# Optimization experiments

Hardware: AMD Instinct MI355X
Metric: run time of the kernel (lower is better)

## Reference

```python
import jax, jax.numpy as jnp
import numpy as np

B, L, M = 32768, 128, 1024  # batch, latent_size, num_basis_function


def setup_inputs() -> dict:
    key = jax.random.key(0)
    k1, k2, k3 = jax.random.split(key, 3)
    u_lat = jax.random.normal(k1, (B, L), dtype=jnp.float32)
    centres = jax.random.normal(k2, (M, L), dtype=jnp.float32)      # RBF centres (torch init: N(0,1))
    log_sigmas = jnp.zeros((M,), dtype=jnp.float32)                  # RBF log bandwidths (torch init: 0)
    lin1_w = jax.random.normal(k3, (M,), dtype=jnp.float32) / np.float32(np.sqrt(M))  # Linear(M,1,bias=False)
    return {"u_lat": u_lat, "centres": centres, "log_sigmas": log_sigmas, "lin1_w": lin1_w}


def _V_batch(u, centres, log_sigmas, lin1_w):
    """Potential V(h) = ELU(w . multiquadric(||h-c||/sigma)) + 0.5*||h||^2, per row. Returns [B]."""
    u_sq = jnp.sum(u * u, axis=-1)                                   # [B]
    c_sq = jnp.sum(centres * centres, axis=-1)                       # [M]
    # ||h - c||^2 via norm expansion: avoids [B, M, L] intermediate
    sq_dist = jnp.maximum(u_sq[:, None] + c_sq[None, :] - 2.0 * (u @ centres.T), 0.0)  # [B, M]
    d = jnp.sqrt(sq_dist) / jnp.exp(log_sigmas)[None, :]             # [B, M]
    phi = jnp.sqrt(1.0 + d * d)                                      # multiquadric kernel
    e = jax.nn.elu(phi @ lin1_w)                                     # [B]
    return e + 0.5 * u_sq


def reference(u_lat, centres, log_sigmas, lin1_w):
    # LEBNN.forward: f_lat = dV/dh evaluated per sample (vmap(jacrev) in torch).
    # Each entry of _V_batch depends only on its own row of u_lat, so
    # grad of the summed potential gives the per-sample Jacobian rows exactly.
    grad_fn = jax.grad(lambda u: jnp.sum(_V_batch(u, centres, log_sigmas, lin1_w)))
    return grad_fn(u_lat)  # [B, L]
```

## Files before the change

### kernel.cpp

```cpp
#include <hip/hip_runtime.h>
#include <math.h>

#define B_N 32768
#define L_N 128
#define M_N 1024
#define NT 512
#define TB 64
#define TM 64
#define NCHUNK (M_N / TM)

typedef __bf16 v8bf __attribute__((ext_vector_type(8)));
typedef __bf16 v4bf __attribute__((ext_vector_type(4)));
typedef float  v4f  __attribute__((ext_vector_type(4)));
typedef float  v2f  __attribute__((ext_vector_type(2)));
typedef unsigned int u32x2 __attribute__((ext_vector_type(2)));

#define MFMA(a, b, c) __builtin_amdgcn_mfma_f32_16x16x32_bf16(a, b, c, 0, 0, 0)

#define US  136
#define CNS 136
#define QSCALE 64.0f
#define QINV   0.015625f

__device__ inline v8bf pack8(float4 a, float4 b) {
    v8bf v;
    v[0] = (__bf16)a.x; v[1] = (__bf16)a.y; v[2] = (__bf16)a.z; v[3] = (__bf16)a.w;
    v[4] = (__bf16)b.x; v[5] = (__bf16)b.y; v[6] = (__bf16)b.z; v[7] = (__bf16)b.w;
    return v;
}

__global__ void lebnn_setup(const float* __restrict__ centres,
                            const float* __restrict__ log_sigmas,
                            const float* __restrict__ lin_w,
                            float4* __restrict__ cpack,
                            __bf16* __restrict__ cT,
                            __bf16* __restrict__ cbn) {
    __shared__ __bf16 tile[64 * 72];
    const int bx = blockIdx.x;
    if (bx < 32) {
        const int m0 = (bx & 15) * 64;
        const int l0 = (bx >> 4) * 64;
        const int row = threadIdx.x >> 2;
        const int seg = threadIdx.x & 3;
        const float* src = centres + (size_t)(m0 + row) * L_N + l0 + seg * 16;
        float4 a0 = *(const float4*)(src);
        float4 a1 = *(const float4*)(src + 4);
        float4 a2 = *(const float4*)(src + 8);
        float4 a3 = *(const float4*)(src + 12);
        v8bf p0 = pack8(a0, a1);
        v8bf p1 = pack8(a2, a3);
        *(v8bf*)&tile[row * 72 + seg * 16]     = p0;
        *(v8bf*)&tile[row * 72 + seg * 16 + 8] = p1;
        __bf16* rdst = cbn + (size_t)(m0 + row) * L_N + l0 + seg * 16;
        *(v8bf*)(rdst)     = p0;
        *(v8bf*)(rdst + 8) = p1;
        __syncthreads();
        v8bf o0, o1;
#pragma unroll
        for (int i = 0; i < 8; ++i) o0[i] = tile[(seg * 16 + i) * 72 + row];
#pragma unroll
        for (int i = 0; i < 8; ++i) o1[i] = tile[(seg * 16 + 8 + i) * 72 + row];
        __bf16* dst = cT + (size_t)(l0 + row) * M_N + m0 + seg * 16;
        *(v8bf*)(dst)     = o0;
        *(v8bf*)(dst + 8) = o1;
    } else {
        int m = (bx - 32) * 256 + threadIdx.x;
        if (m < M_N) {
            const float4* row = (const float4*)(centres + (size_t)m * L_N);
            float s = 0.f;
#pragma unroll
            for (int i = 0; i < L_N / 4; ++i) {
                float4 v = row[i];
                s += v.x * v.x + v.y * v.y + v.z * v.z + v.w * v.w;
            }
            float4 p;
            p.x = s;
            p.y = expf(-2.f * log_sigmas[m]);
            p.z = lin_w[m];
            p.w = 0.f;
            cpack[m] = p;
        }
    }
}

__global__ __launch_bounds__(NT) void lebnn_phase1(
    const float* __restrict__ u, const __bf16* __restrict__ cbn,
    const float4* __restrict__ cpack, unsigned int* __restrict__ qg32,
    float* __restrict__ gg, float* __restrict__ rsg)
{
    __shared__ __bf16 u_bf[TB * US];
    __shared__ __bf16 c_n[TM * CNS];
    __shared__ float usq_s[TB];
    __shared__ float upart[TB * 9];
    __shared__ float sred[288];
    __shared__ float rred[288];

    const int tid  = threadIdx.x;
    const int w    = tid >> 6;
    const int lane = tid & 63;
    const int l15  = lane & 15;
    const int l4   = lane >> 4;
    const int bh   = w >> 2;
    const int mq   = w & 3;
    const int b0   = blockIdx.x * TB;

    {
        int row = tid >> 3, seg = tid & 7;
        const float* up = u + (size_t)(b0 + row) * L_N + seg * 16;
        float4 a0 = *(const float4*)(up);
        float4 a1 = *(const float4*)(up + 4);
        float4 a2 = *(const float4*)(up + 8);
        float4 a3 = *(const float4*)(up + 12);
        float ps = a0.x*a0.x + a0.y*a0.y + a0.z*a0.z + a0.w*a0.w
                 + a1.x*a1.x + a1.y*a1.y + a1.z*a1.z + a1.w*a1.w
                 + a2.x*a2.x + a2.y*a2.y + a2.z*a2.z + a2.w*a2.w
                 + a3.x*a3.x + a3.y*a3.y + a3.z*a3.z + a3.w*a3.w;
        *(v8bf*)&u_bf[row * US + seg * 16]     = pack8(a0, a1);
        *(v8bf*)&u_bf[row * US + seg * 16 + 8] = pack8(a2, a3);
        upart[row * 9 + seg] = ps;
    }
    __syncthreads();
    if (tid < TB) {
        float s = 0.f;
#pragma unroll
        for (int i = 0; i < 8; ++i) s += upart[tid * 9 + i];
        usq_s[tid] = s;
    }
    __syncthreads();

    v8bf uf[2][4];
#pragma unroll
    for (int bt = 0; bt < 2; ++bt)
#pragma unroll
        for (int kk = 0; kk < 4; ++kk)
            uf[bt][kk] = *(v8bf*)&u_bf[(bh*32 + bt*16 + l15) * US + kk*32 + l4*8];

    float usq_r[2][4];
#pragma unroll
    for (int bt = 0; bt < 2; ++bt)
#pragma unroll
        for (int r = 0; r < 4; ++r)
            usq_r[bt][r] = usq_s[bh*32 + bt*16 + l4*4 + r];

    float s_p[2][4] = {{0.f,0.f,0.f,0.f},{0.f,0.f,0.f,0.f}};
    float r_p[2][4] = {{0.f,0.f,0.f,0.f},{0.f,0.f,0.f,0.f}};

    const int srow = tid >> 3;
    const int sseg = tid & 7;

    for (int mt = 0; mt < NCHUNK; ++mt) {
        const int m0 = mt * TM;
        __syncthreads();
        {
            const __bf16* cp = cbn + (size_t)(m0 + srow) * L_N + sseg * 16;
            *(v8bf*)&c_n[srow * CNS + sseg * 16]     = *(const v8bf*)(cp);
            *(v8bf*)&c_n[srow * CNS + sseg * 16 + 8] = *(const v8bf*)(cp + 8);
        }
        float4 cpv = cpack[m0 + mq*16 + l15];
        __syncthreads();

        v4f dot[2];
        dot[0] = (v4f){0.f,0.f,0.f,0.f};
        dot[1] = (v4f){0.f,0.f,0.f,0.f};
#pragma unroll
        for (int kk = 0; kk < 4; ++kk) {
            v8bf bfr = *(v8bf*)&c_n[(mq*16 + l15) * CNS + kk*32 + l4*8];
            dot[0] = MFMA(uf[0][kk], bfr, dot[0]);
            dot[1] = MFMA(uf[1][kk], bfr, dot[1]);
        }

        float qs[8];
        const float wqs = cpv.z * cpv.y * QSCALE;
#pragma unroll
        for (int bt = 0; bt < 2; ++bt) {
#pragma unroll
            for (int r = 0; r < 4; ++r) {
                float dv  = dot[bt][r];
                float raw = fmaf(-2.f, dv, usq_r[bt][r] + cpv.x);
                float x   = fmaf(fmaxf(raw, 0.f), cpv.y, 1.f);
                float ri  = rsqrtf(x);
                s_p[bt][r] = fmaf(cpv.z, x * ri, s_p[bt][r]);
                float qv  = (raw > 0.f) ? wqs * ri : 0.f;
                r_p[bt][r] += qv;
                qs[bt*4 + r] = qv;
            }
        }
        unsigned int w0 = 0, w1 = 0;
        w0 = __builtin_amdgcn_cvt_pk_fp8_f32(qs[0], qs[1], w0, false);
        w0 = __builtin_amdgcn_cvt_pk_fp8_f32(qs[2], qs[3], w0, true);
        w1 = __builtin_amdgcn_cvt_pk_fp8_f32(qs[4], qs[5], w1, false);
        w1 = __builtin_amdgcn_cvt_pk_fp8_f32(qs[6], qs[7], w1, true);
        u32x2 qw; qw[0] = w0; qw[1] = w1;
        *(u32x2*)(qg32 + ((size_t)blockIdx.x * NCHUNK + mt) * (NT * 2) + tid * 2) = qw;
    }

#pragma unroll
    for (int bt = 0; bt < 2; ++bt)
#pragma unroll
        for (int r = 0; r < 4; ++r) {
#pragma unroll
            for (int msk = 1; msk < 16; msk <<= 1) {
                s_p[bt][r] += __shfl_xor(s_p[bt][r], msk, 64);
                r_p[bt][r] += __shfl_xor(r_p[bt][r], msk, 64);
            }
        }
    if (l15 == 0) {
#pragma unroll
        for (int bt = 0; bt < 2; ++bt)
#pragma unroll
            for (int r = 0; r < 4; ++r) {
                sred[w*36 + bt*16 + l4*4 + r] = s_p[bt][r];
                rred[w*36 + bt*16 + l4*4 + r] = r_p[bt][r];
            }
    }
    __syncthreads();

    if (tid < TB) {
        int bhh = tid >> 5, rowr = tid & 31;
        float s = 0.f, R = 0.f;
#pragma unroll
        for (int i = 0; i < 4; ++i) {
            s += sred[(bhh*4 + i)*36 + rowr];
            R += rred[(bhh*4 + i)*36 + rowr];
        }
        float g = (s > 0.f) ? 1.f : expf(s);
        gg[b0 + tid]  = g;
        rsg[b0 + tid] = fmaf(g * QINV, R, 1.f);
    }
}

__global__ __launch_bounds__(NT) void lebnn_gemm2(
    const float* __restrict__ u, const unsigned int* __restrict__ qg32,
    const __bf16* __restrict__ cT, const float* __restrict__ gg,
    const float* __restrict__ rsg, float* __restrict__ out)
{
    __shared__ __bf16 qt[64 * 72];
    __shared__ __bf16 ct[128 * 72];

    const int tid  = threadIdx.x;
    const int w    = tid >> 6;
    const int lane = tid & 63;
    const int l15  = lane & 15;
    const int l4   = lane >> 4;
    const int bh   = w >> 2;
    const int lq   = w & 3;
    const int bb0  = blockIdx.x * 64;
    const int lr   = tid >> 2;
    const int sg   = tid & 3;

    v4f acc[2][2];
#pragma unroll
    for (int bt = 0; bt < 2; ++bt)
#pragma unroll
        for (int lt = 0; lt < 2; ++lt)
            acc[bt][lt] = (v4f){0.f, 0.f, 0.f, 0.f};

    u32x2 qw = *(const u32x2*)(qg32 + ((size_t)blockIdx.x * NCHUNK + 0) * (NT * 2) + tid * 2);
    const __bf16* csrc = cT + (size_t)lr * M_N + sg * 16;
    v8bf cva = *(const v8bf*)(csrc);
    v8bf cvb = *(const v8bf*)(csrc + 8);

    for (int mt = 0; mt < NCHUNK; ++mt) {
        __syncthreads();
        {
            v2f p0 = __builtin_amdgcn_cvt_pk_f32_fp8(qw[0], false);
            v2f p1 = __builtin_amdgcn_cvt_pk_f32_fp8(qw[0], true);
            v2f p2 = __builtin_amdgcn_cvt_pk_f32_fp8(qw[1], false);
            v2f p3 = __builtin_amdgcn_cvt_pk_f32_fp8(qw[1], true);
            __bf16 qb[8];
            qb[0] = (__bf16)p0[0]; qb[1] = (__bf16)p0[1];
            qb[2] = (__bf16)p1[0]; qb[3] = (__bf16)p1[1];
            qb[4] = (__bf16)p2[0]; qb[5] = (__bf16)p2[1];
            qb[6] = (__bf16)p3[0]; qb[7] = (__bf16)p3[1];
#pragma unroll
            for (int bt = 0; bt < 2; ++bt)
#pragma unroll
                for (int r = 0; r < 4; ++r)
                    qt[(bh*32 + bt*16 + l4*4 + r) * 72 + lq*16 + l15] = qb[bt*4 + r];
            *(v8bf*)&ct[lr * 72 + sg * 16]     = cva;
            *(v8bf*)&ct[lr * 72 + sg * 16 + 8] = cvb;
        }
        __syncthreads();

        if (mt + 1 < NCHUNK) {
            qw = *(const u32x2*)(qg32 + ((size_t)blockIdx.x * NCHUNK + (mt+1)) * (NT * 2) + tid * 2);
            const __bf16* cn = cT + (size_t)lr * M_N + (mt+1) * TM + sg * 16;
            cva = *(const v8bf*)(cn);
            cvb = *(const v8bf*)(cn + 8);
        }

#pragma unroll
        for (int kk = 0; kk < 2; ++kk) {
            v8bf qa0 = *(v8bf*)&qt[(bh*32 +  0 + l15) * 72 + kk*32 + l4*8];
            v8bf qa1 = *(v8bf*)&qt[(bh*32 + 16 + l15) * 72 + kk*32 + l4*8];
#pragma unroll
            for (int lt = 0; lt < 2; ++lt) {
                v8bf cb = *(v8bf*)&ct[(lq*32 + lt*16 + l15) * 72 + kk*32 + l4*8];
                acc[0][lt] = MFMA(qa0, cb, acc[0][lt]);
                acc[1][lt] = MFMA(qa1, cb, acc[1][lt]);
            }
        }
    }

    float gv[2][4], rv[2][4];
#pragma unroll
    for (int bt = 0; bt < 2; ++bt)
#pragma unroll
        for (int r = 0; r < 4; ++r) {
            int b = bb0 + bh*32 + bt*16 + l4*4 + r;
            gv[bt][r] = gg[b] * QINV;
            rv[bt][r] = rsg[b];
        }
#pragma unroll
    for (int bt = 0; bt < 2; ++bt)
#pragma unroll
        for (int lt = 0; lt < 2; ++lt)
#pragma unroll
            for (int r = 0; r < 4; ++r) {
                size_t idx = (size_t)(bb0 + bh*32 + bt*16 + l4*4 + r) * L_N
                           + lq*32 + lt*16 + l15;
                out[idx] = fmaf(u[idx], rv[bt][r], -gv[bt][r] * acc[bt][lt][r]);
            }
}

#define CFS 68
#define OFF_UBF   0
#define OFF_CN    17408
#define OFF_CFL   34816
#define OFF_USQ   52224
#define OFF_UPART 52480
#define OFF_SRED  54784
#define OFF_RRED  55936
#define OFF_G     57088
#define OFF_RS    57344
#define SMEM_BYTES 57600

__global__ __launch_bounds__(NT) void lebnn_fallback(
    const float* __restrict__ u, const float* __restrict__ centres,
    const float4* __restrict__ cpack, float* __restrict__ out)
{
    extern __shared__ char smem[];
    __bf16* u_bf = (__bf16*)(smem + OFF_UBF);
    __bf16* c_n  = (__bf16*)(smem + OFF_CN);
    float*  cfl  = (float*)(smem + OFF_CFL);
    float* usq_s = (float*)(smem + OFF_USQ);
    float* upart = (float*)(smem + OFF_UPART);
    float* sred  = (float*)(smem + OFF_SRED);
    float* rred  = (float*)(smem + OFF_RRED);
    float* gsh   = (float*)(smem + OFF_G);
    float* rssh  = (float*)(smem + OFF_RS);

    const int tid  = threadIdx.x;
    const int w    = tid >> 6;
    const int lane = tid & 63;
    const int l15  = lane & 15;
    const int l4   = lane >> 4;
    const int bh   = w >> 2;
    const int mq   = w & 3;
    const int tx   = tid & 15;
    const int ty   = tid >> 4;
    const int b0   = blockIdx.x * 64;

    {
        int row = tid >> 3, seg = tid & 7;
        const float* up = u + (size_t)(b0 + row) * L_N + seg * 16;
        float4 a0 = *(const float4*)(up);
        float4 a1 = *(const float4*)(up + 4);
        float4 a2 = *(const float4*)(up + 8);
        float4 a3 = *(const float4*)(up + 12);
        float ps = a0.x*a0.x + a0.y*a0.y + a0.z*a0.z + a0.w*a0.w
                 + a1.x*a1.x + a1.y*a1.y + a1.z*a1.z + a1.w*a1.w
                 + a2.x*a2.x + a2.y*a2.y + a2.z*a2.z + a2.w*a2.w
                 + a3.x*a3.x + a3.y*a3.y + a3.z*a3.z + a3.w*a3.w;
        *(v8bf*)&u_bf[row * US + seg * 16]     = pack8(a0, a1);
        *(v8bf*)&u_bf[row * US + seg * 16 + 8] = pack8(a2, a3);
        upart[row * 9 + seg] = ps;
    }
    __syncthreads();
    if (tid < 64) {
        float s = 0.f;
#pragma unroll
        for (int i = 0; i < 8; ++i) s += upart[tid * 9 + i];
        usq_s[tid] = s;
    }
    __syncthreads();

    v8bf uf[2][4];
#pragma unroll
    for (int bt = 0; bt < 2; ++bt)
#pragma unroll
        for (int kk = 0; kk < 4; ++kk)
            uf[bt][kk] = *(v8bf*)&u_bf[(bh*32 + bt*16 + l15) * US + kk*32 + l4*8];

    float usq_r[2][4];
#pragma unroll
    for (int bt = 0; bt < 2; ++bt)
#pragma unroll
        for (int r = 0; r < 4; ++r)
            usq_r[bt][r] = usq_s[bh*32 + bt*16 + l4*4 + r];

    float s_p[2][4] = {{0.f,0.f,0.f,0.f},{0.f,0.f,0.f,0.f}};
    float r_p[2][4] = {{0.f,0.f,0.f,0.f},{0.f,0.f,0.f,0.f}};
    float T[4][4] = {{0.f}};

    const int rp = tid >> 4;
    const int cg = tid & 15;

    for (int mt = 0; mt < NCHUNK; ++mt) {
        const int m0 = mt * TM;
        __syncthreads();
        {
            const float* cp0 = centres + (size_t)(m0 + 2*rp) * L_N + cg * 8;
            float4 r0a = *(const float4*)(cp0);
            float4 r0b = *(const float4*)(cp0 + 4);
            float4 r1a = *(const float4*)(cp0 + L_N);
            float4 r1b = *(const float4*)(cp0 + L_N + 4);
            *(v8bf*)&c_n[(2*rp)     * CNS + cg*8] = pack8(r0a, r0b);
            *(v8bf*)&c_n[(2*rp + 1) * CNS + cg*8] = pack8(r1a, r1b);
        }
        float4 cpv = cpack[m0 + mq*16 + l15];
        __syncthreads();

        v4f dot[2];
        dot[0] = (v4f){0.f,0.f,0.f,0.f};
        dot[1] = (v4f){0.f,0.f,0.f,0.f};
#pragma unroll
        for (int kk = 0; kk < 4; ++kk) {
            v8bf bfr = *(v8bf*)&c_n[(mq*16 + l15) * CNS + kk*32 + l4*8];
            dot[0] = MFMA(uf[0][kk], bfr, dot[0]);
            dot[1] = MFMA(uf[1][kk], bfr, dot[1]);
        }

#pragma unroll
        for (int bt = 0; bt < 2; ++bt) {
#pragma unroll
            for (int r = 0; r < 4; ++r) {
                float dv  = dot[bt][r];
                float raw = fmaf(-2.f, dv, usq_r[bt][r] + cpv.x);
                float x   = fmaf(fmaxf(raw, 0.f), cpv.y, 1.f);
                float ri  = rsqrtf(x);
                s_p[bt][r] = fmaf(cpv.z, x * ri, s_p[bt][r]);
                float qv  = (raw > 0.f) ? cpv.z * cpv.y * ri : 0.f;
                r_p[bt][r] += qv;
                cfl[(mq*16 + l15) * CFS + bh*32 + bt*16 + l4*4 + r] = qv;
            }
        }
        __syncthreads();

        for (int mm = 0; mm < TM; ++mm) {
            v4f cf = *(v4f*)&cfl[mm * CFS + tx*4];
            v4bf cb = *(v4bf*)&c_n[mm * CNS + ty*4];
            float cv[4] = {(float)cb[0], (float)cb[1], (float)cb[2], (float)cb[3]};
#pragma unroll
            for (int i = 0; i < 4; ++i)
#pragma unroll
                for (int j = 0; j < 4; ++j)
                    T[i][j] = fmaf(cf[i], cv[j], T[i][j]);
        }
    }

    __syncthreads();

#pragma unroll
    for (int bt = 0; bt < 2; ++bt)
#pragma unroll
        for (int r = 0; r < 4; ++r) {
#pragma unroll
            for (int msk = 1; msk < 16; msk <<= 1) {
                s_p[bt][r] += __shfl_xor(s_p[bt][r], msk, 64);
                r_p[bt][r] += __shfl_xor(r_p[bt][r], msk, 64);
            }
        }
    if (l15 == 0) {
#pragma unroll
        for (int bt = 0; bt < 2; ++bt)
#pragma unroll
            for (int r = 0; r < 4; ++r) {
                sred[w*36 + bt*16 + l4*4 + r] = s_p[bt][r];
                rred[w*36 + bt*16 + l4*4 + r] = r_p[bt][r];
            }
    }
    __syncthreads();

    if (tid < 64) {
        int bhh = tid >> 5, rowr = tid & 31;
        float s = 0.f, R = 0.f;
#pragma unroll
        for (int i = 0; i < 4; ++i) {
            s += sred[(bhh*4 + i)*36 + rowr];
            R += rred[(bhh*4 + i)*36 + rowr];
        }
        float g = (s > 0.f) ? 1.f : expf(s);
        gsh[tid]  = g;
        rssh[tid] = fmaf(g, R, 1.f);
    }
    __syncthreads();

#pragma unroll
    for (int i = 0; i < 4; ++i) {
        int b = tx*4 + i;
        float rv = rssh[b];
        float gv = gsh[b];
        size_t idx = (size_t)(b0 + b) * L_N + ty*4;
        float4 uu = *(const float4*)(u + idx);
        float4 o;
        o.x = fmaf(uu.x, rv, -gv * T[i][0]);
        o.y = fmaf(uu.y, rv, -gv * T[i][1]);
        o.z = fmaf(uu.z, rv, -gv * T[i][2]);
        o.w = fmaf(uu.w, rv, -gv * T[i][3]);
        *(float4*)(out + idx) = o;
    }
}

extern "C" void kernel_launch(void* const* d_in, const int* in_sizes, int n_in,
                              void* d_out, int out_size, void* d_ws, size_t ws_size,
                              hipStream_t stream) {
    const float* u          = (const float*)d_in[0];
    const float* centres    = (const float*)d_in[1];
    const float* log_sigmas = (const float*)d_in[2];
    const float* lin_w      = (const float*)d_in[3];
    float* out = (float*)d_out;

    char* wsb = (char*)d_ws;
    float4* cpack = (float4*)wsb;
    __bf16* cT    = (__bf16*)(wsb + 16384);
    __bf16* cbn   = (__bf16*)(wsb + 278528);
    float*  gg    = (float*) (wsb + 540672);
    float*  rsg   = (float*) (wsb + 671744);
    unsigned int* qg32 = (unsigned int*)(wsb + 802816);
    const size_t WS_NEED = 802816ULL + 33554432ULL;

    lebnn_setup<<<36, 256, 0, stream>>>(centres, log_sigmas, lin_w, cpack, cT, cbn);

    if (ws_size >= WS_NEED) {
        lebnn_phase1<<<B_N / TB, NT, 0, stream>>>(u, cbn, cpack, qg32, gg, rsg);
        lebnn_gemm2<<<B_N / 64, NT, 0, stream>>>(u, qg32, cT, gg, rsg, out);
    } else {
        hipFuncSetAttribute((const void*)lebnn_fallback,
                            hipFuncAttributeMaxDynamicSharedMemorySize, SMEM_BYTES);
        lebnn_fallback<<<B_N / 64, NT, SMEM_BYTES, stream>>>(u, centres, cpack, out);
    }
}
```

Before: 63.35 us.

## Register-prefetch centres in gemm1 and load gemm2 B operands directly from global

```diff
diff --git a/kernel.cpp b/kernel.cpp
--- a/kernel.cpp
+++ b/kernel.cpp
@@ -148,16 +148,26 @@
     const int srow = tid >> 3;
     const int sseg = tid & 7;
 
+    v8bf lda, ldb;
+    {
+        const __bf16* cp = cbn + (size_t)srow * L_N + sseg * 16;
+        lda = *(const v8bf*)(cp);
+        ldb = *(const v8bf*)(cp + 8);
+    }
+
     for (int mt = 0; mt < NCHUNK; ++mt) {
         const int m0 = mt * TM;
         __syncthreads();
-        {
-            const __bf16* cp = cbn + (size_t)(m0 + srow) * L_N + sseg * 16;
-            *(v8bf*)&c_n[srow * CNS + sseg * 16]     = *(const v8bf*)(cp);
-            *(v8bf*)&c_n[srow * CNS + sseg * 16 + 8] = *(const v8bf*)(cp + 8);
-        }
+        *(v8bf*)&c_n[srow * CNS + sseg * 16]     = lda;
+        *(v8bf*)&c_n[srow * CNS + sseg * 16 + 8] = ldb;
         float4 cpv = cpack[m0 + mq*16 + l15];
         __syncthreads();
+
+        if (mt + 1 < NCHUNK) {
+            const __bf16* cp = cbn + (size_t)((mt+1)*TM + srow) * L_N + sseg * 16;
+            lda = *(const v8bf*)(cp);
+            ldb = *(const v8bf*)(cp + 8);
+        }
 
         v4f dot[2];
         dot[0] = (v4f){0.f,0.f,0.f,0.f};
@@ -235,7 +245,6 @@
     const float* __restrict__ rsg, float* __restrict__ out)
 {
     __shared__ __bf16 qt[64 * 72];
-    __shared__ __bf16 ct[128 * 72];
 
     const int tid  = threadIdx.x;
     const int w    = tid >> 6;
@@ -245,8 +254,6 @@
     const int bh   = w >> 2;
     const int lq   = w & 3;
     const int bb0  = blockIdx.x * 64;
-    const int lr   = tid >> 2;
-    const int sg   = tid & 3;
 
     v4f acc[2][2];
 #pragma unroll
@@ -255,49 +262,82 @@
         for (int lt = 0; lt < 2; ++lt)
             acc[bt][lt] = (v4f){0.f, 0.f, 0.f, 0.f};
 
-    u32x2 qw = *(const u32x2*)(qg32 + ((size_t)blockIdx.x * NCHUNK + 0) * (NT * 2) + tid * 2);
-    const __bf16* csrc = cT + (size_t)lr * M_N + sg * 16;
-    v8bf cva = *(const v8bf*)(csrc);
-    v8bf cvb = *(const v8bf*)(csrc + 8);
-
-    for (int mt = 0; mt < NCHUNK; ++mt) {
-        __syncthreads();
+    const size_t qbase = (size_t)blockIdx.x * NCHUNK;
+    const __bf16* crow0 = cT + (size_t)(lq*32 +  0 + l15) * M_N + l4*8;
+    const __bf16* crow1 = cT + (size_t)(lq*32 + 16 + l15) * M_N + l4*8;
+
+    u32x2 qwA = *(const u32x2*)(qg32 + qbase * (NT*2) + tid*2);
+    u32x2 qwB;
+    v8bf cbA0 = *(const v8bf*)(crow0);
+    v8bf cbA1 = *(const v8bf*)(crow1);
+    v8bf cbA2 = *(const v8bf*)(crow0 + 32);
+    v8bf cbA3 = *(const v8bf*)(crow1 + 32);
+    v8bf cbB0, cbB1, cbB2, cbB3;
+
+#define SCATTER_Q(QW)                                                        \
+    {                                                                        \
+        v2f p0 = __builtin_amdgcn_cvt_pk_f32_fp8((QW)[0], false);            \
+        v2f p1 = __builtin_amdgcn_cvt_pk_f32_fp8((QW)[0], true);             \
+        v2f p2 = __builtin_amdgcn_cvt_pk_f32_fp8((QW)[1], false);            \
+        v2f p3 = __builtin_amdgcn_cvt_pk_f32_fp8((QW)[1], true);             \
+        __bf16 qb[8];                                                        \
+        qb[0] = (__bf16)p0[0]; qb[1] = (__bf16)p0[1];                        \
+        qb[2] = (__bf16)p1[0]; qb[3] = (__bf16)p1[1];                        \
+        qb[4] = (__bf16)p2[0]; qb[5] = (__bf16)p2[1];                        \
+        qb[6] = (__bf16)p3[0]; qb[7] = (__bf16)p3[1];                        \
+        _Pragma("unroll")                                                    \
+        for (int bt = 0; bt < 2; ++bt)                                       \
+            _Pragma("unroll")                                                \
+            for (int r = 0; r < 4; ++r)                                      \
+                qt[(bh*32 + bt*16 + l4*4 + r) * 72 + lq*16 + l15] = qb[bt*4 + r]; \
+    }
+
+#define MFMA_CHUNK(CB0, CB1, CB2, CB3)                                       \
+    {                                                                        \
+        v8bf qa0 = *(v8bf*)&qt[(bh*32 +  0 + l15) * 72 +  0 + l4*8];         \
+        v8bf qa1 = *(v8bf*)&qt[(bh*32 + 16 + l15) * 72 +  0 + l4*8];         \
+        acc[0][0] = MFMA(qa0, CB0, acc[0][0]);                               \
+        acc[0][1] = MFMA(qa0, CB1, acc[0][1]);                               \
+        acc[1][0] = MFMA(qa1, CB0, acc[1][0]);                               \
+        acc[1][1] = MFMA(qa1, CB1, acc[1][1]);                               \
+        qa0 = *(v8bf*)&qt[(bh*32 +  0 + l15) * 72 + 32 + l4*8];              \
+        qa1 = *(v8bf*)&qt[(bh*32 + 16 + l15) * 72 + 32 + l4*8];              \
+        acc[0][0] = MFMA(qa0, CB2, acc[0][0]);                               \
+        acc[0][1] = MFMA(qa0, CB3, acc[0][1]);                               \
+        acc[1][0] = MFMA(qa1, CB2, acc[1][0]);                               \
+        acc[1][1] = MFMA(qa1, CB3, acc[1][1]);                               \
+    }
+
+    SCATTER_Q(qwA);
+    __syncthreads();
+
+    for (int mt = 0; mt < NCHUNK; mt += 2) {
         {
-            v2f p0 = __builtin_amdgcn_cvt_pk_f32_fp8(qw[0], false);
-            v2f p1 = __builtin_amdgcn_cvt_pk_f32_fp8(qw[0], true);
-            v2f p2 = __builtin_amdgcn_cvt_pk_f32_fp8(qw[1], false);
-            v2f p3 = __builtin_amdgcn_cvt_pk_f32_fp8(qw[1], true);
-            __bf16 qb[8];
-            qb[0] = (__bf16)p0[0]; qb[1] = (__bf16)p0[1];
-            qb[2] = (__bf16)p1[0]; qb[3] = (__bf16)p1[1];
-            qb[4] = (__bf16)p2[0]; qb[5] = (__bf16)p2[1];
-            qb[6] = (__bf16)p3[0]; qb[7] = (__bf16)p3[1];
-#pragma unroll
-            for (int bt = 0; bt < 2; ++bt)
-#pragma unroll
-                for (int r = 0; r < 4; ++r)
-                    qt[(bh*32 + bt*16 + l4*4 + r) * 72 + lq*16 + l15] = qb[bt*4 + r];
-            *(v8bf*)&ct[lr * 72 + sg * 16]     = cva;
-            *(v8bf*)&ct[lr * 72 + sg * 16 + 8] = cvb;
-        }
-        __syncthreads();
-
-        if (mt + 1 < NCHUNK) {
-            qw = *(const u32x2*)(qg32 + ((size_t)blockIdx.x * NCHUNK + (mt+1)) * (NT * 2) + tid * 2);
-            const __bf16* cn = cT + (size_t)lr * M_N + (mt+1) * TM + sg * 16;
-            cva = *(const v8bf*)(cn);
-            cvb = *(const v8bf*)(cn + 8);
-        }
-
-#pragma unroll
-        for (int kk = 0; kk < 2; ++kk) {
-            v8bf qa0 = *(v8bf*)&qt[(bh*32 +  0 + l15) * 72 + kk*32 + l4*8];
-            v8bf qa1 = *(v8bf*)&qt[(bh*32 + 16 + l15) * 72 + kk*32 + l4*8];
-#pragma unroll
-            for (int lt = 0; lt < 2; ++lt) {
-                v8bf cb = *(v8bf*)&ct[(lq*32 + lt*16 + l15) * 72 + kk*32 + l4*8];
-                acc[0][lt] = MFMA(qa0, cb, acc[0][lt]);
-                acc[1][lt] = MFMA(qa1, cb, acc[1][lt]);
+            const int c1 = mt + 1;
+            qwB  = *(const u32x2*)(qg32 + (qbase + c1) * (NT*2) + tid*2);
+            cbB0 = *(const v8bf*)(crow0 + c1*64);
+            cbB1 = *(const v8bf*)(crow1 + c1*64);
+            cbB2 = *(const v8bf*)(crow0 + c1*64 + 32);
+            cbB3 = *(const v8bf*)(crow1 + c1*64 + 32);
+            MFMA_CHUNK(cbA0, cbA1, cbA2, cbA3);
+            __syncthreads();
+            SCATTER_Q(qwB);
+            __syncthreads();
+        }
+        {
+            const int c2 = mt + 2;
+            if (c2 < NCHUNK) {
+                qwA  = *(const u32x2*)(qg32 + (qbase + c2) * (NT*2) + tid*2);
+                cbA0 = *(const v8bf*)(crow0 + c2*64);
+                cbA1 = *(const v8bf*)(crow1 + c2*64);
+                cbA2 = *(const v8bf*)(crow0 + c2*64 + 32);
+                cbA3 = *(const v8bf*)(crow1 + c2*64 + 32);
+            }
+            MFMA_CHUNK(cbB0, cbB1, cbB2, cbB3);
+            if (c2 < NCHUNK) {
+                __syncthreads();
+                SCATTER_Q(qwA);
+                __syncthreads();
             }
         }
     }
@@ -321,6 +361,8 @@
                            + lq*32 + lt*16 + l15;
                 out[idx] = fmaf(u[idx], rv[bt][r], -gv[bt][r] * acc[bt][lt][r]);
             }
+#undef SCATTER_Q
+#undef MFMA_CHUNK
 }
 
 #define CFS 68
```

Result: slower. 74.48 us (+17.6%).
